# Kernel tuning notes

Measured on AMD Instinct MI355X. Metric: run time of the kernel, lower is better.

## Reference

```python
import jax, jax.numpy as jnp
import numpy as np
from jax import lax

B, C_IN, HC, H, W, K = 32, 32, 64, 64, 64, 3


def _conv(x, w, b):
    # x: [B,C,H,W], w: [O,I,K,K] -> [B,O,H,W] (stride 1, pad 1)
    y = lax.conv_general_dilated(x, w, window_strides=(1, 1), padding=[(1, 1), (1, 1)],
                                 dimension_numbers=("NCHW", "OIHW", "NCHW"))
    return y + b[None, :, None, None]


def setup_inputs() -> dict:
    key = jax.random.key(0)
    ks = jax.random.split(key, 20)
    d = {
        "x": jax.random.normal(ks[0], (B, C_IN, H, W), jnp.float32),
        "hidden_state": jax.random.normal(ks[1], (B, HC, H, W), jnp.float32),
        "cell_state": jax.random.normal(ks[2], (B, HC, H, W), jnp.float32),
    }
    sx = 1.0 / np.sqrt(C_IN * K * K)
    sh = 1.0 / np.sqrt(HC * K * K)
    names_x = ["w_xi", "w_xf", "w_xo", "w_xg"]
    names_h = ["w_hi", "w_hf", "w_ho", "w_hg"]
    for i, n in enumerate(names_x):
        d[n] = jax.random.uniform(ks[3 + i], (HC, C_IN, K, K), jnp.float32, -sx, sx)
        d["b" + n[1:]] = jax.random.uniform(ks[7 + i], (HC,), jnp.float32, -sx, sx)
    for i, n in enumerate(names_h):
        d[n] = jax.random.uniform(ks[11 + i], (HC, HC, K, K), jnp.float32, -sh, sh)
        d["b" + n[1:]] = jax.random.uniform(ks[15 + i], (HC,), jnp.float32, -sh, sh)
    return d


def reference(x, hidden_state, cell_state,
              w_xi, w_xf, w_xo, w_xg, b_xi, b_xf, b_xo, b_xg,
              w_hi, w_hf, w_ho, w_hg, b_hi, b_hf, b_ho, b_hg):
    Wx = jnp.concatenate([w_xi, w_xf, w_xo, w_xg], axis=0)
    bx = jnp.concatenate([b_xi, b_xf, b_xo, b_xg], axis=0)
    Wh = jnp.concatenate([w_hi, w_hf, w_ho, w_hg], axis=0)
    bh = jnp.concatenate([b_hi, b_hf, b_ho, b_hg], axis=0)
    gates = _conv(x, Wx, bx) + _conv(hidden_state, Wh, bh)  # [B,4*HC,H,W]
    zi, zf, zo, zg = jnp.split(gates, 4, axis=1)
    i = jax.nn.sigmoid(zi)
    f = jax.nn.sigmoid(zf)
    o = jax.nn.sigmoid(zo)
    g = jnp.tanh(zg)
    c_new = f * cell_state + i * g
    h_new = o * jnp.tanh(c_new)
    return (h_new, c_new)
```

## Files before the change

kernel.cpp:

```cpp
#include <hip/hip_runtime.h>


#define B_   32
#define CIN  32
#define HC_  64
#define HH   64
#define WW   64

#define A_ELEMS (9 * 6 * 8 * 64 * 8)
#define P_ROW   (12 * 66 * 8)
#define CHUNK   12288

typedef __attribute__((ext_vector_type(8)))  short  short8;
typedef __attribute__((ext_vector_type(16))) float  floatx16;

struct PackArgs {
    const float* wx[4]; const float* wh[4];
    const float* bx[4]; const float* bh[4];
};

__device__ __forceinline__ short f2bf(float f) {
    unsigned u = __float_as_uint(f);
    u += 0x7FFFu + ((u >> 16) & 1u);
    return (short)(u >> 16);
}

__device__ __forceinline__ void gl_lds16(const short* g, short* l) {
    __builtin_amdgcn_global_load_lds(
        (const __attribute__((address_space(1))) unsigned int*)g,
        (__attribute__((address_space(3))) unsigned int*)l, 16, 0, 0);
}

__global__ __launch_bounds__(256) void pack_weights(PackArgs pa, short* a_pk, float* bias) {
    int idx = blockIdx.x * 256 + threadIdx.x;
    if (idx < A_ELEMS) {
        int j    = idx & 7;
        int lane = (idx >> 3) & 63;
        int rest = idx >> 9;
        int s    = rest & 7;
        int rest2 = rest >> 3;
        int kk   = rest2 % 6;
        int tap  = rest2 / 6;
        int og = s >> 1, fi = s & 1;
        int m32 = lane & 31;
        int gate = 2 * fi + (m32 >> 4);
        int oc   = og * 16 + (m32 & 15);
        int c    = kk * 16 + (lane >> 5) * 8 + j;
        int ky = tap / 3, kx = tap - 3 * ky;
        float v = (c < CIN)
            ? pa.wx[gate][((oc * CIN + c) * 3 + ky) * 3 + kx]
            : pa.wh[gate][((oc * HC_ + (c - CIN)) * 3 + ky) * 3 + kx];
        a_pk[idx] = f2bf(v);
    }
    if (idx < 256) {
        int gate = idx >> 6, oc = idx & 63;
        bias[idx] = pa.bx[gate][oc] + pa.bh[gate][oc];
    }
}

__global__ __launch_bounds__(256) void pack_input(const float* __restrict__ x,
                                                  const float* __restrict__ h,
                                                  short* __restrict__ P) {
    const int yy = blockIdx.x, b = blockIdx.y;
    int4* prow4 = (int4*)(P + ((size_t)b * 66 + yy) * P_ROW);

    if (yy == 0 || yy == 65) {
        int4 z = {0, 0, 0, 0};
        for (int g = threadIdx.x; g < 792; g += 256) prow4[g] = z;
        return;
    }

    __shared__ short t[64 * 98];
    const int y = yy - 1;
    const int col = threadIdx.x & 63, cg = threadIdx.x >> 6;
    for (int c = cg; c < 96; c += 4) {
        float v = (c < CIN) ? x[((b * CIN + c) * HH + y) * WW + col]
                            : h[((b * HC_ + (c - CIN)) * HH + y) * WW + col];
        t[col * 98 + c] = f2bf(v);
    }
    __syncthreads();

    for (int g = threadIdx.x; g < 792; g += 256) {
        int pc = g / 66, xx = g - 66 * pc;
        int4 val = {0, 0, 0, 0};
        if (xx >= 1 && xx <= 64) {
            const short* sp = &t[(xx - 1) * 98 + pc * 8];
            val.x = *(const int*)(sp + 0); val.y = *(const int*)(sp + 2);
            val.z = *(const int*)(sp + 4); val.w = *(const int*)(sp + 6);
        }
        prow4[g] = val;
    }
}

__global__ __launch_bounds__(512, 4) void convlstm_main(
    const short* __restrict__ P, const short* __restrict__ a_pk,
    const float* __restrict__ bias, const float* __restrict__ cell,
    float* __restrict__ out)
{
    __shared__ __align__(16) short As[2][CHUNK];

    const int tid = threadIdx.x;
    const int b  = blockIdx.x >> 5;
    const int y0 = (blockIdx.x & 31) * 2;

    const int wv = tid >> 6, lane = tid & 63;
    const int ln31 = lane & 31, hg = lane >> 5;
    const int og = wv & 3, nh = wv >> 2;
    const int y = y0 + nh;

    floatx16 acc[2][2];
    #pragma unroll
    for (int fi = 0; fi < 2; ++fi)
        #pragma unroll
        for (int ns = 0; ns < 2; ++ns)
            #pragma unroll
            for (int q = 0; q < 16; ++q) acc[fi][ns][q] = 0.f;

    const int a_base = og * 1024 + lane * 8;
    const int lnoff  = (hg * 66 + ln31) * 8;

    {
        const short* src = a_pk;
        #pragma unroll
        for (int i = 0; i < 3; ++i)
            gl_lds16(src + (i * 512 + tid) * 8, &As[0][(i * 512 + wv * 64) * 8]);
    }
    __syncthreads();

    #pragma unroll
    for (int c = 0; c < 18; ++c) {
        const int cur = c & 1;
        if (c < 17) {
            const short* src = a_pk + (c + 1) * CHUNK;
            #pragma unroll
            for (int i = 0; i < 3; ++i)
                gl_lds16(src + (i * 512 + tid) * 8,
                         &As[cur ^ 1][(i * 512 + wv * 64) * 8]);
        }

        const int tap = c >> 1, half = c & 1;
        const int ky = tap / 3, kx = tap % 3;
        const short* Brow = P + ((size_t)(b * 66) + y + ky) * P_ROW + kx * 8 + lnoff;
        const short* Ac = As[cur];

        #pragma unroll
        for (int kkl = 0; kkl < 3; ++kkl) {
            const int kkg = half * 3 + kkl;
            short8 a0 = *(const short8*)&Ac[a_base + kkl * 4096];
            short8 a1 = *(const short8*)&Ac[a_base + kkl * 4096 + 512];
            short8 b0 = *(const short8*)&Brow[(2 * kkg * 66 + 0 ) * 8];
            short8 b1 = *(const short8*)&Brow[(2 * kkg * 66 + 32) * 8];
            acc[0][0] = __builtin_amdgcn_mfma_f32_32x32x16_bf16(a0, b0, acc[0][0], 0, 0, 0);
            acc[0][1] = __builtin_amdgcn_mfma_f32_32x32x16_bf16(a0, b1, acc[0][1], 0, 0, 0);
            acc[1][0] = __builtin_amdgcn_mfma_f32_32x32x16_bf16(a1, b0, acc[1][0], 0, 0, 0);
            acc[1][1] = __builtin_amdgcn_mfma_f32_32x32x16_bf16(a1, b1, acc[1][1], 0, 0, 0);
        }
        __syncthreads();
    }

    const size_t plane = (size_t)B_ * HC_ * HH * WW;
    #pragma unroll
    for (int q = 0; q < 4; ++q)
    #pragma unroll
    for (int b8 = 0; b8 < 2; ++b8) {
        const int oc16 = q + 4 * hg + 8 * b8;
        const int oc = og * 16 + oc16;
        const float Bi = bias[oc],       Bf = bias[64 + oc];
        const float Bo = bias[128 + oc], Bg = bias[192 + oc];
        const int r_lo = q + 4 * b8, r_hi = q + 4 * (2 + b8);
        #pragma unroll
        for (int ns = 0; ns < 2; ++ns) {
            float zi = acc[0][ns][r_lo] + Bi;
            float zf = acc[0][ns][r_hi] + Bf;
            float zo = acc[1][ns][r_lo] + Bo;
            float zg = acc[1][ns][r_hi] + Bg;
            float ig = 1.f / (1.f + __expf(-zi));
            float fg = 1.f / (1.f + __expf(-zf));
            float sg = 1.f / (1.f + __expf(-zo));
            float e2 = __expf(2.f * zg);
            float gg = 1.f - 2.f / (e2 + 1.f);
            const int x = ns * 32 + ln31;
            size_t off = ((size_t)(b * HC_ + oc) * HH + y) * WW + x;
            float cn = fg * cell[off] + ig * gg;
            float ec = __expf(2.f * cn);
            out[off] = sg * (1.f - 2.f / (ec + 1.f));
            out[plane + off] = cn;
        }
    }
}

extern "C" void kernel_launch(void* const* d_in, const int* in_sizes, int n_in,
                              void* d_out, int out_size, void* d_ws, size_t ws_size,
                              hipStream_t stream) {
    PackArgs pa;
    pa.wx[0] = (const float*)d_in[3];  pa.bx[0] = (const float*)d_in[4];
    pa.wx[1] = (const float*)d_in[5];  pa.bx[1] = (const float*)d_in[6];
    pa.wx[2] = (const float*)d_in[7];  pa.bx[2] = (const float*)d_in[8];
    pa.wx[3] = (const float*)d_in[9];  pa.bx[3] = (const float*)d_in[10];
    pa.wh[0] = (const float*)d_in[11]; pa.bh[0] = (const float*)d_in[12];
    pa.wh[1] = (const float*)d_in[13]; pa.bh[1] = (const float*)d_in[14];
    pa.wh[2] = (const float*)d_in[15]; pa.bh[2] = (const float*)d_in[16];
    pa.wh[3] = (const float*)d_in[17]; pa.bh[3] = (const float*)d_in[18];

    short* a_pk = (short*)d_ws;
    float* bias = (float*)((char*)d_ws + A_ELEMS * sizeof(short));
    short* P    = (short*)((char*)d_ws + 443392);

    pack_weights<<<dim3(A_ELEMS / 256), dim3(256), 0, stream>>>(pa, a_pk, bias);
    pack_input <<<dim3(66, B_), dim3(256), 0, stream>>>(
        (const float*)d_in[0], (const float*)d_in[1], P);
    convlstm_main<<<dim3(B_ * 32), dim3(512), 0, stream>>>(
        P, a_pk, bias, (const float*)d_in[2], (float*)d_out);
}
```

Baseline: 231.8 us.

## Stage input rows in LDS and triple-buffer weight slices per k-step

The input tile (4 padded rows of the packed activation buffer) is loaded once into LDS with global_load_lds, so B operands come from LDS instead of repeated global reads. Weights now stream in 54 small per-k slices through a 3-deep ring buffer, with manual vmcnt waits and raw barriers replacing __syncthreads. This cuts redundant global traffic for activations across the 9 taps. The cost is a barrier on every k-step and a larger LDS footprint, which may lower occupancy.

```diff
diff --git a/kernel.cpp b/kernel.cpp
--- a/kernel.cpp
+++ b/kernel.cpp
@@ -9,7 +9,8 @@
 
 #define A_ELEMS (9 * 6 * 8 * 64 * 8)
 #define P_ROW   (12 * 66 * 8)
-#define CHUNK   12288
+#define AKK     4096
+#define BLDS    25344
 
 typedef __attribute__((ext_vector_type(8)))  short  short8;
 typedef __attribute__((ext_vector_type(16))) float  floatx16;
@@ -97,7 +98,7 @@
     const float* __restrict__ bias, const float* __restrict__ cell,
     float* __restrict__ out)
 {
-    __shared__ __align__(16) short As[2][CHUNK];
+    __shared__ __align__(16) short lds[BLDS + 3 * AKK];
 
     const int tid = threadIdx.x;
     const int b  = blockIdx.x >> 5;
@@ -116,46 +117,52 @@
             #pragma unroll
             for (int q = 0; q < 16; ++q) acc[fi][ns][q] = 0.f;
 
-    const int a_base = og * 1024 + lane * 8;
-    const int lnoff  = (hg * 66 + ln31) * 8;
+    short* Asl = lds + BLDS;
+    const int a_rd  = og * 1024 + lane * 8;
+    const int b_rd  = nh * 6336 + hg * 528 + ln31 * 8;
 
     {
-        const short* src = a_pk;
+        const short* Bsrc = P + ((size_t)(b * 66) + y0) * P_ROW;
         #pragma unroll
-        for (int i = 0; i < 3; ++i)
-            gl_lds16(src + (i * 512 + tid) * 8, &As[0][(i * 512 + wv * 64) * 8]);
-    }
-    __syncthreads();
-
-    #pragma unroll
-    for (int c = 0; c < 18; ++c) {
-        const int cur = c & 1;
-        if (c < 17) {
-            const short* src = a_pk + (c + 1) * CHUNK;
-            #pragma unroll
-            for (int i = 0; i < 3; ++i)
-                gl_lds16(src + (i * 512 + tid) * 8,
-                         &As[cur ^ 1][(i * 512 + wv * 64) * 8]);
-        }
-
-        const int tap = c >> 1, half = c & 1;
+        for (int i = 0; i < 7; ++i) {
+            int id = i * 512 + tid;
+            if (id < 3168)
+                gl_lds16(Bsrc + id * 8, lds + (i * 512 + wv * 64) * 8);
+        }
+        gl_lds16(a_pk + tid * 8,       Asl + wv * 64 * 8);
+        gl_lds16(a_pk + AKK + tid * 8, Asl + AKK + wv * 64 * 8);
+    }
+    asm volatile("s_waitcnt vmcnt(1)" ::: "memory");
+    __builtin_amdgcn_s_barrier();
+    __builtin_amdgcn_sched_barrier(0);
+
+    #pragma unroll
+    for (int c = 0; c < 54; ++c) {
+        const int tap = c / 6, kk = c % 6;
         const int ky = tap / 3, kx = tap % 3;
-        const short* Brow = P + ((size_t)(b * 66) + y + ky) * P_ROW + kx * 8 + lnoff;
-        const short* Ac = As[cur];
-
-        #pragma unroll
-        for (int kkl = 0; kkl < 3; ++kkl) {
-            const int kkg = half * 3 + kkl;
-            short8 a0 = *(const short8*)&Ac[a_base + kkl * 4096];
-            short8 a1 = *(const short8*)&Ac[a_base + kkl * 4096 + 512];
-            short8 b0 = *(const short8*)&Brow[(2 * kkg * 66 + 0 ) * 8];
-            short8 b1 = *(const short8*)&Brow[(2 * kkg * 66 + 32) * 8];
-            acc[0][0] = __builtin_amdgcn_mfma_f32_32x32x16_bf16(a0, b0, acc[0][0], 0, 0, 0);
-            acc[0][1] = __builtin_amdgcn_mfma_f32_32x32x16_bf16(a0, b1, acc[0][1], 0, 0, 0);
-            acc[1][0] = __builtin_amdgcn_mfma_f32_32x32x16_bf16(a1, b0, acc[1][0], 0, 0, 0);
-            acc[1][1] = __builtin_amdgcn_mfma_f32_32x32x16_bf16(a1, b1, acc[1][1], 0, 0, 0);
-        }
-        __syncthreads();
+
+        if (c < 52)
+            gl_lds16(a_pk + (c + 2) * AKK + tid * 8,
+                     Asl + ((c + 2) % 3) * AKK + wv * 64 * 8);
+
+        const short* Ab = Asl + (c % 3) * AKK;
+        const short* Bb = lds + b_rd + ky * 6336 + kk * 1056 + kx * 8;
+
+        short8 a0 = *(const short8*)&Ab[a_rd];
+        short8 a1 = *(const short8*)&Ab[a_rd + 512];
+        short8 b0 = *(const short8*)&Bb[0];
+        short8 b1 = *(const short8*)&Bb[256];
+        acc[0][0] = __builtin_amdgcn_mfma_f32_32x32x16_bf16(a0, b0, acc[0][0], 0, 0, 0);
+        acc[0][1] = __builtin_amdgcn_mfma_f32_32x32x16_bf16(a0, b1, acc[0][1], 0, 0, 0);
+        acc[1][0] = __builtin_amdgcn_mfma_f32_32x32x16_bf16(a1, b0, acc[1][0], 0, 0, 0);
+        acc[1][1] = __builtin_amdgcn_mfma_f32_32x32x16_bf16(a1, b1, acc[1][1], 0, 0, 0);
+
+        if (c < 52)       asm volatile("s_waitcnt vmcnt(1)" ::: "memory");
+        else if (c == 52) asm volatile("s_waitcnt vmcnt(0)" ::: "memory");
+        if (c < 53) {
+            __builtin_amdgcn_s_barrier();
+            __builtin_amdgcn_sched_barrier(0);
+        }
     }
 
     const size_t plane = (size_t)B_ * HC_ * HH * WW;
```

After: 222.6 us. -4.0%, faster.
